# Optimization experiments

Measured on AMD Instinct MI355X. Metric: run time of the kernel, lower is better.

The kernel has to match this reference:

```python
import jax, jax.numpy as jnp
import numpy as np

NUM_Q_HEADS = 32
NUM_KV_HEADS = 8
HEAD_DIM = 128
HIDDEN = 4096
EPS = 1e-6
ROPE_THETA = 1e6


def _rmsnorm(t, w):
    # per-head RMSNorm over last dim (head_dim), as in skip_rmsnorm with residual=None
    var = jnp.mean(t * t, axis=-1, keepdims=True)
    return t * jax.lax.rsqrt(var + EPS) * w


def _rotate_half(t):
    h = t.shape[-1] // 2
    return jnp.concatenate([-t[..., h:], t[..., :h]], axis=-1)


def setup_inputs() -> dict:
    key = jax.random.key(0)
    ks = jax.random.split(key, 4)
    B, S = 2, 1024
    x = jax.random.normal(ks[0], (B, S, HIDDEN), jnp.float32)
    q_proj_w = jax.random.normal(ks[1], (HIDDEN, NUM_Q_HEADS * HEAD_DIM), jnp.float32) * 0.02
    kv_proj_w = jax.random.normal(ks[2], (HIDDEN, 2 * NUM_KV_HEADS * HEAD_DIM), jnp.float32) * 0.02
    o_proj_w = jax.random.normal(ks[3], (NUM_Q_HEADS * HEAD_DIM, HIDDEN), jnp.float32) * 0.02
    q_norm_w = jnp.ones((HEAD_DIM,), jnp.float32)
    k_norm_w = jnp.ones((HEAD_DIM,), jnp.float32)
    # real rotate-half RoPE tables, shape [S, head_dim]
    inv_freq = 1.0 / (ROPE_THETA ** (jnp.arange(0, HEAD_DIM, 2, dtype=jnp.float32) / HEAD_DIM))
    freqs = jnp.arange(S, dtype=jnp.float32)[:, None] * inv_freq[None, :]  # [S, hd/2]
    emb = jnp.concatenate([freqs, freqs], axis=-1)  # [S, hd]
    cos, sin = jnp.cos(emb), jnp.sin(emb)
    kv_buffer = jnp.zeros((16384, 2 * NUM_KV_HEADS, HEAD_DIM), jnp.float32)
    cur_select_index = jnp.arange(B * S, dtype=jnp.int32)
    return {"x": x, "q_proj_w": q_proj_w, "kv_proj_w": kv_proj_w, "o_proj_w": o_proj_w,
            "q_norm_w": q_norm_w, "k_norm_w": k_norm_w, "cos": cos, "sin": sin,
            "kv_buffer": kv_buffer, "cur_select_index": cur_select_index}


def reference(x, q_proj_w, kv_proj_w, o_proj_w, q_norm_w, k_norm_w, cos, sin, kv_buffer, cur_select_index):
    B, S, _ = x.shape
    T = B * S
    xf = x.reshape(T, HIDDEN)
    # projections (weights stored as [in, out])
    xq = (xf @ q_proj_w).reshape(T, NUM_Q_HEADS, HEAD_DIM)
    xkv = xf @ kv_proj_w
    xk = xkv[:, : NUM_KV_HEADS * HEAD_DIM].reshape(T, NUM_KV_HEADS, HEAD_DIM)
    xv = xkv[:, NUM_KV_HEADS * HEAD_DIM:].reshape(T, NUM_KV_HEADS, HEAD_DIM)
    # per-head RMSNorm (Qwen3 q/k norm)
    xq = _rmsnorm(xq, q_norm_w)
    xk = _rmsnorm(xk, k_norm_w)
    # RoPE (cos/sin are [S, hd], tiled over batch, broadcast over heads)
    cos_t = jnp.tile(cos, (B, 1))[:, None, :]  # [T,1,hd]
    sin_t = jnp.tile(sin, (B, 1))[:, None, :]
    xq = xq * cos_t + _rotate_half(xq) * sin_t
    xk = xk * cos_t + _rotate_half(xk) * sin_t
    # paged KV-cache scatter update (update_kv_buffer)
    combined_kv = jnp.concatenate([xk, xv], axis=1)  # [T, 2*Hk, hd]
    buf = kv_buffer.at[cur_select_index].set(combined_kv)
    # ragged causal flash attention (equal per-request lengths here), GQA expand
    rep = NUM_Q_HEADS // NUM_KV_HEADS
    q = xq.reshape(B, S, NUM_Q_HEADS, HEAD_DIM)
    k = jnp.repeat(xk.reshape(B, S, NUM_KV_HEADS, HEAD_DIM), rep, axis=2)
    v = jnp.repeat(xv.reshape(B, S, NUM_KV_HEADS, HEAD_DIM), rep, axis=2)
    scale = HEAD_DIM ** -0.5
    scores = jnp.einsum('bqhd,bkhd->bhqk', q, k) * scale  # [B,H,S,S]
    causal = jnp.tril(jnp.ones((S, S), bool))
    scores = jnp.where(causal[None, None], scores, jnp.float32(-1e30))
    p = jax.nn.softmax(scores, axis=-1)
    attn = jnp.einsum('bhqk,bkhd->bqhd', p, v).reshape(B, S, NUM_Q_HEADS * HEAD_DIM)
    out = attn @ o_proj_w  # [B,S,hidden]
    return out, buf
```

## Files before the change

kernel.cpp:

```cpp
#include <hip/hip_runtime.h>

typedef float fx4 __attribute__((ext_vector_type(4)));
typedef short s16x4 __attribute__((ext_vector_type(4)));
typedef short s16x8 __attribute__((ext_vector_type(8)));
typedef __bf16 bf16x8 __attribute__((ext_vector_type(8)));

__device__ __forceinline__ short f2bf(float f) {
  unsigned u = __builtin_bit_cast(unsigned, f);
  u += 0x7fffu + ((u >> 16) & 1u);
  return (short)(u >> 16);
}

__device__ __forceinline__ bf16x8 ld8(const short* p) {
  s16x8 v = *(const s16x8*)p;
  return __builtin_bit_cast(bf16x8, v);
}

__device__ __forceinline__ void gld16(const void* g, void* l) {
  __builtin_amdgcn_global_load_lds(
      (const __attribute__((address_space(1))) unsigned*)g,
      (__attribute__((address_space(3))) unsigned*)l, 16, 0, 0);
}

template<int N> __device__ __forceinline__ void wait_vmcnt() {
  if constexpr (N == 0)      asm volatile("s_waitcnt vmcnt(0)" ::: "memory");
  else if constexpr (N == 4) asm volatile("s_waitcnt vmcnt(4)" ::: "memory");
  else if constexpr (N == 6) asm volatile("s_waitcnt vmcnt(6)" ::: "memory");
  __builtin_amdgcn_sched_barrier(0);
}

__device__ __forceinline__ void barrier_pin() {
  __builtin_amdgcn_s_barrier();
  __builtin_amdgcn_sched_barrier(0);
}

__global__ __launch_bounds__(256) void cvt_k(const float* __restrict__ in,
                                             short* __restrict__ out) {
  int i = (blockIdx.x * 256 + threadIdx.x) * 8;
  fx4 a = *(const fx4*)(in + i);
  fx4 b = *(const fx4*)(in + i + 4);
  s16x8 w;
  w[0] = f2bf(a[0]); w[1] = f2bf(a[1]); w[2] = f2bf(a[2]); w[3] = f2bf(a[3]);
  w[4] = f2bf(b[0]); w[5] = f2bf(b[1]); w[6] = f2bf(b[2]); w[7] = f2bf(b[3]);
  *(s16x8*)(out + i) = w;
}

__global__ __launch_bounds__(256) void tr_k(const float* __restrict__ in,
    short* __restrict__ out, int K, int N) {
  __shared__ short T[64][72];
  const int ktiles = K >> 6;
  const int tk0 = (blockIdx.x % ktiles) << 6;
  const int tn0 = (blockIdx.x / ktiles) << 6;
  const int tid = threadIdx.x;
  #pragma unroll
  for (int i = 0; i < 4; ++i) {
    int idx = i * 256 + tid;
    int k = idx >> 4, n4 = (idx & 15) << 2;
    fx4 v = *(const fx4*)(in + (size_t)(tk0 + k) * N + tn0 + n4);
    #pragma unroll
    for (int j = 0; j < 4; ++j) T[n4 + j][k] = f2bf(v[j]);
  }
  __syncthreads();
  #pragma unroll
  for (int i = 0; i < 2; ++i) {
    int idx = i * 256 + tid;
    int n = idx >> 3, k8 = (idx & 7) << 3;
    *(s16x8*)(out + (size_t)(tn0 + n) * K + tk0 + k8) = *(const s16x8*)&T[n][k8];
  }
}

__global__ __launch_bounds__(256) void vtr_k(const short* __restrict__ vbp,
                                             short* __restrict__ vbt) {
  __shared__ short T[64][72];
  const int tile = blockIdx.x & 31;
  const int tt = tile & 15, dt = tile >> 4;
  const int bk = blockIdx.x >> 5;
  const int b = bk >> 3, kvh = bk & 7;
  const int t0 = tt << 6, d0 = dt << 6;
  const int tid = threadIdx.x;
  #pragma unroll
  for (int i = 0; i < 2; ++i) {
    int idx = i * 256 + tid;
    int r = idx >> 3, c8 = (idx & 7) << 3;
    s16x8 v = *(const s16x8*)(vbp + (size_t)(b * 1024 + t0 + r) * 1024 + kvh * 128 + d0 + c8);
    #pragma unroll
    for (int j = 0; j < 8; ++j) T[c8 + j][r] = v[j];
  }
  __syncthreads();
  #pragma unroll
  for (int i = 0; i < 2; ++i) {
    int idx = i * 256 + tid;
    int r = idx >> 3, c8 = (idx & 7) << 3;
    *(s16x8*)(vbt + ((size_t)(b * 8 + kvh) * 128 + d0 + r) * 1024 + t0 + c8) =
        *(const s16x8*)&T[r][c8];
  }
}

__global__ __launch_bounds__(512) void gemm8(const short* __restrict__ A,
    const short* __restrict__ Bt, float* __restrict__ Cp, int N, int K) {
  __shared__ short As[2][2][128 * 64];
  __shared__ short Bs[2][2][128 * 64];
  const int tiles_n = N >> 8;
  const int tm = blockIdx.x / tiles_n, tn = blockIdx.x % tiles_n;
  const int tid = threadIdx.x;
  const int lane = tid & 63, wv = tid >> 6;
  const int wm = (wv >> 2) << 6;
  const int wn = (wv & 3) << 5;
  const int r0 = tm << 8, c0 = tn << 8;
  const int lrow = lane & 15, lg = lane >> 4;

  auto stageA = [&](int t, int hh) {
    int k0 = t << 6, s = t & 1;
    #pragma unroll
    for (int i = 0; i < 2; ++i) {
      int c = i * 512 + tid;
      int row = c >> 3, ch = c & 7;
      gld16(A + (size_t)(r0 + hh * 128 + row) * K + k0 + ((ch ^ (row & 7)) << 3),
            &As[s][hh][(i * 512 + wv * 64) * 8]);
    }
  };
  auto stageB = [&](int t, int hh) {
    int k0 = t << 6, s = t & 1;
    #pragma unroll
    for (int i = 0; i < 2; ++i) {
      int c = i * 512 + tid;
      int row = c >> 3, ch = c & 7;
      gld16(Bt + (size_t)(c0 + hh * 128 + row) * K + k0 + ((ch ^ (row & 7)) << 3),
            &Bs[s][hh][(i * 512 + wv * 64) * 8]);
    }
  };

  fx4 acc[2][2][4][2] = {};
  bf16x8 a[4][2], b[2][2];

  auto ldA = [&](int s, int hh) {
    #pragma unroll
    for (int mf = 0; mf < 4; ++mf) {
      int lr = wm + mf * 16 + lrow;
      #pragma unroll
      for (int ks = 0; ks < 2; ++ks)
        a[mf][ks] = ld8(&As[s][hh][lr * 64 + ((((ks << 2) + lg) ^ (lr & 7)) << 3)]);
    }
  };
  auto ldB = [&](int s, int hh) {
    #pragma unroll
    for (int nf = 0; nf < 2; ++nf) {
      int lr = wn + nf * 16 + lrow;
      #pragma unroll
      for (int ks = 0; ks < 2; ++ks)
        b[nf][ks] = ld8(&Bs[s][hh][lr * 64 + ((((ks << 2) + lg) ^ (lr & 7)) << 3)]);
    }
  };

  const int nt = K >> 6;
  stageA(0, 0); stageA(0, 1); stageB(0, 0); stageB(0, 1);
  stageA(1, 0); stageB(1, 1);

  for (int t = 0; t < nt; ++t) {
    const int s = t & 1;
    if (t + 1 < nt) wait_vmcnt<4>(); else wait_vmcnt<0>();
    barrier_pin();
    ldA(s, 0); ldB(s, 0);
    if (t + 1 < nt) stageA(t + 1, 1);
    __builtin_amdgcn_s_setprio(1);
    #pragma unroll
    for (int ks = 0; ks < 2; ++ks)
      #pragma unroll
      for (int mf = 0; mf < 4; ++mf)
        #pragma unroll
        for (int nf = 0; nf < 2; ++nf)
          acc[0][0][mf][nf] = __builtin_amdgcn_mfma_f32_16x16x32_bf16(
              a[mf][ks], b[nf][ks], acc[0][0][mf][nf], 0, 0, 0);
    __builtin_amdgcn_s_setprio(0);
    barrier_pin();
    ldB(s, 1);
    if (t + 1 < nt) stageB(t + 1, 0);
    __builtin_amdgcn_s_setprio(1);
    #pragma unroll
    for (int ks = 0; ks < 2; ++ks)
      #pragma unroll
      for (int mf = 0; mf < 4; ++mf)
        #pragma unroll
        for (int nf = 0; nf < 2; ++nf)
          acc[0][1][mf][nf] = __builtin_amdgcn_mfma_f32_16x16x32_bf16(
              a[mf][ks], b[nf][ks], acc[0][1][mf][nf], 0, 0, 0);
    __builtin_amdgcn_s_setprio(0);
    barrier_pin();
    ldA(s, 1);
    if (t + 2 < nt) stageA(t + 2, 0);
    __builtin_amdgcn_s_setprio(1);
    #pragma unroll
    for (int ks = 0; ks < 2; ++ks)
      #pragma unroll
      for (int mf = 0; mf < 4; ++mf)
        #pragma unroll
        for (int nf = 0; nf < 2; ++nf)
          acc[1][1][mf][nf] = __builtin_amdgcn_mfma_f32_16x16x32_bf16(
              a[mf][ks], b[nf][ks], acc[1][1][mf][nf], 0, 0, 0);
    __builtin_amdgcn_s_setprio(0);
    barrier_pin();
    ldB(s, 0);
    if (t + 2 < nt) stageB(t + 2, 1);
    __builtin_amdgcn_s_setprio(1);
    #pragma unroll
    for (int ks = 0; ks < 2; ++ks)
      #pragma unroll
      for (int mf = 0; mf < 4; ++mf)
        #pragma unroll
        for (int nf = 0; nf < 2; ++nf)
          acc[1][0][mf][nf] = __builtin_amdgcn_mfma_f32_16x16x32_bf16(
              a[mf][ks], b[nf][ks], acc[1][0][mf][nf], 0, 0, 0);
    __builtin_amdgcn_s_setprio(0);
    barrier_pin();
  }
  const int g4 = lg << 2;
  #pragma unroll
  for (int mq = 0; mq < 2; ++mq)
    #pragma unroll
    for (int nq = 0; nq < 2; ++nq)
      #pragma unroll
      for (int mf = 0; mf < 4; ++mf)
        #pragma unroll
        for (int nf = 0; nf < 2; ++nf)
          #pragma unroll
          for (int j = 0; j < 4; ++j) {
            int row = r0 + mq * 128 + wm + mf * 16 + g4 + j;
            int col = c0 + nq * 128 + wn + nf * 16 + lrow;
            Cp[(size_t)row * N + col] = acc[mq][nq][mf][nf][j];
          }
}

__global__ __launch_bounds__(512) void gemm4(const short* __restrict__ A,
    const short* __restrict__ Bt, float* __restrict__ Cp, int N, int K) {
  __shared__ short As[3][2][128 * 64];
  __shared__ short Bs[3][128 * 64];
  const int tiles_n = N >> 7;
  const int tm = blockIdx.x / tiles_n, tn = blockIdx.x % tiles_n;
  const int tid = threadIdx.x;
  const int lane = tid & 63, wv = tid >> 6;
  const int wm = (wv >> 2) << 6;
  const int wn = (wv & 3) << 5;
  const int r0 = tm << 8, c0 = tn << 7;
  const int lrow = lane & 15, lg = lane >> 4;

  auto stageA = [&](int t, int hh) {
    int k0 = t << 6, s = t % 3;
    #pragma unroll
    for (int i = 0; i < 2; ++i) {
      int c = i * 512 + tid;
      int row = c >> 3, ch = c & 7;
      gld16(A + (size_t)(r0 + hh * 128 + row) * K + k0 + ((ch ^ (row & 7)) << 3),
            &As[s][hh][(i * 512 + wv * 64) * 8]);
    }
  };
  auto stageB = [&](int t) {
    int k0 = t << 6, s = t % 3;
    #pragma unroll
    for (int i = 0; i < 2; ++i) {
      int c = i * 512 + tid;
      int row = c >> 3, ch = c & 7;
      gld16(Bt + (size_t)(c0 + row) * K + k0 + ((ch ^ (row & 7)) << 3),
            &Bs[s][(i * 512 + wv * 64) * 8]);
    }
  };

  fx4 acc[2][4][2] = {};
  bf16x8 a[4][2], b[2][2];

  auto ldA = [&](int s, int hh) {
    #pragma unroll
    for (int mf = 0; mf < 4; ++mf) {
      int lr = wm + mf * 16 + lrow;
      #pragma unroll
      for (int ks = 0; ks < 2; ++ks)
        a[mf][ks] = ld8(&As[s][hh][lr * 64 + ((((ks << 2) + lg) ^ (lr & 7)) << 3)]);
    }
  };
  auto ldB = [&](int s) {
    #pragma unroll
    for (int nf = 0; nf < 2; ++nf) {
      int lr = wn + nf * 16 + lrow;
      #pragma unroll
      for (int ks = 0; ks < 2; ++ks)
        b[nf][ks] = ld8(&Bs[s][lr * 64 + ((((ks << 2) + lg) ^ (lr & 7)) << 3)]);
    }
  };

  const int nt = K >> 6;
  stageA(0, 0); stageA(0, 1); stageB(0);
  stageA(1, 0); stageA(1, 1); stageB(1);

  for (int t = 0; t < nt; ++t) {
    const int s = t % 3;
    if (t + 1 < nt) wait_vmcnt<6>(); else wait_vmcnt<0>();
    barrier_pin();
    ldA(s, 0); ldB(s);
    if (t + 2 < nt) stageA(t + 2, 0);
    __builtin_amdgcn_s_setprio(1);
    #pragma unroll
    for (int ks = 0; ks < 2; ++ks)
      #pragma unroll
      for (int mf = 0; mf < 4; ++mf)
        #pragma unroll
        for (int nf = 0; nf < 2; ++nf)
          acc[0][mf][nf] = __builtin_amdgcn_mfma_f32_16x16x32_bf16(
              a[mf][ks], b[nf][ks], acc[0][mf][nf], 0, 0, 0);
    __builtin_amdgcn_s_setprio(0);
    barrier_pin();
    ldA(s, 1);
    if (t + 2 < nt) { stageA(t + 2, 1); stageB(t + 2); }
    __builtin_amdgcn_s_setprio(1);
    #pragma unroll
    for (int ks = 0; ks < 2; ++ks)
      #pragma unroll
      for (int mf = 0; mf < 4; ++mf)
        #pragma unroll
        for (int nf = 0; nf < 2; ++nf)
          acc[1][mf][nf] = __builtin_amdgcn_mfma_f32_16x16x32_bf16(
              a[mf][ks], b[nf][ks], acc[1][mf][nf], 0, 0, 0);
    __builtin_amdgcn_s_setprio(0);
    barrier_pin();
  }
  const int g4 = lg << 2;
  #pragma unroll
  for (int mh = 0; mh < 2; ++mh)
    #pragma unroll
    for (int mf = 0; mf < 4; ++mf)
      #pragma unroll
      for (int nf = 0; nf < 2; ++nf)
        #pragma unroll
        for (int j = 0; j < 4; ++j) {
          int row = r0 + mh * 128 + wm + mf * 16 + g4 + j;
          int col = c0 + wn + nf * 16 + lrow;
          Cp[(size_t)row * N + col] = acc[mh][mf][nf][j];
        }
}

__global__ __launch_bounds__(256) void nr_k(const float* __restrict__ xqkv,
    const float* __restrict__ qnw, const float* __restrict__ knw,
    const float* __restrict__ cosb, const float* __restrict__ sinb,
    const int* __restrict__ idx,
    short* __restrict__ qb, short* __restrict__ kbp, short* __restrict__ vbp,
    float* __restrict__ bufo) {
  int rid = blockIdx.x * 4 + (threadIdx.x >> 6);
  int l = threadIdx.x & 63;
  int type, t, h;
  if (rid < 65536)      { type = 0; t = rid >> 5; h = rid & 31; }
  else if (rid < 81920) { type = 1; int r = rid - 65536; t = r >> 3; h = r & 7; }
  else                  { type = 2; int r = rid - 81920; t = r >> 3; h = r & 7; }
  int s = t & 1023;
  const float* src = xqkv + (size_t)t * 6144 +
                     ((type == 0) ? h * 128 : (type == 1) ? 4096 + h * 128
                                                          : 5120 + h * 128);
  float e0 = src[l], e1 = src[l + 64];
  float out0, out1;
  if (type < 2) {
    float ss = e0 * e0 + e1 * e1;
    #pragma unroll
    for (int off = 1; off < 64; off <<= 1) ss += __shfl_xor(ss, off);
    float r = rsqrtf(ss * (1.0f / 128.0f) + 1e-6f);
    const float* nw = (type == 0) ? qnw : knw;
    float n0 = e0 * r * nw[l], n1 = e1 * r * nw[l + 64];
    float c0 = cosb[s * 128 + l], c1 = cosb[s * 128 + 64 + l];
    float s0 = sinb[s * 128 + l], s1 = sinb[s * 128 + 64 + l];
    out0 = n0 * c0 - n1 * s0;
    out1 = n1 * c1 + n0 * s1;
  } else { out0 = e0; out1 = e1; }
  if (type == 0) {
    short* d = qb + (size_t)t * 4096 + h * 128;
    d[l] = f2bf(out0); d[l + 64] = f2bf(out1);
  } else {
    int br = idx[t];
    float* bd = bufo + (size_t)br * 2048 + (type == 1 ? 0 : 1024) + h * 128;
    bd[l] = out0; bd[l + 64] = out1;
    short* d = (type == 1) ? kbp + (size_t)t * 1024 + h * 128
                           : vbp + (size_t)t * 1024 + h * 128;
    d[l] = f2bf(out0); d[l + 64] = f2bf(out1);
  }
}

#define KLD 136
#define PLD 72

__global__ __launch_bounds__(256) void attn_k(const short* __restrict__ qb,
    const short* __restrict__ kbp, const short* __restrict__ vbt,
    short* __restrict__ ob) {
  __shared__ short Ks[64 * KLD];
  __shared__ short Vs[128 * 64];
  __shared__ short Ps[4][16 * PLD];
  const int bid = blockIdx.x;
  const int qt = 15 - (bid & 15), h = (bid >> 4) & 31, b = bid >> 9;
  const int kvh = h >> 2;
  const int tid = threadIdx.x, lane = tid & 63, w = tid >> 6;
  const int lrow = lane & 15, lg = lane >> 4, lk = lg << 3;
  const int q0 = qt << 6;
  const float SC2 = 0.088388347648318447f * 1.4426950408889634f;

  bf16x8 qf[4];
  {
    const short* qp = qb + ((size_t)(b * 1024 + q0 + w * 16 + lrow) * 32 + h) * 128 + lk;
    #pragma unroll
    for (int kb4 = 0; kb4 < 4; ++kb4) qf[kb4] = ld8(qp + kb4 * 32);
  }

  const short* vt_base = vbt + (size_t)(b * 8 + kvh) * 128 * 1024;

  const int sr = tid >> 4, sd8 = (tid & 15) << 3;
  const int vdr = tid >> 3, vch = tid & 7;
  s16x8 kreg[4], vreg[4];
  auto ldkv = [&](int kv0) {
    #pragma unroll
    for (int it = 0; it < 4; ++it) {
      int r = (it << 4) + sr;
      kreg[it] = *(const s16x8*)(kbp + ((size_t)(b * 1024 + kv0 + r) * 8 + kvh) * 128 + sd8);
      int d = (it << 5) + vdr;
      vreg[it] = *(const s16x8*)(vt_base + (size_t)d * 1024 + kv0 + (vch << 3));
    }
  };
  auto wrkv = [&]() {
    #pragma unroll
    for (int it = 0; it < 4; ++it) {
      int r = (it << 4) + sr;
      *(s16x8*)&Ks[r * KLD + sd8] = kreg[it];
      int d = (it << 5) + vdr;
      *(s16x8*)&Vs[d * 64 + ((vch ^ (d & 7)) << 3)] = vreg[it];
    }
  };

  float m[4], lsum[4];
  fx4 acc[8] = {};
  #pragma unroll
  for (int j = 0; j < 4; ++j) { m[j] = -3.0e38f; lsum[j] = 0.f; }

  ldkv(0);
  wrkv();
  __syncthreads();

  for (int kt = 0; kt <= qt; ++kt) {
    const int kv0 = kt << 6;
    if (kt < qt) ldkv((kt + 1) << 6);
    fx4 sf[4];
    #pragma unroll
    for (int nc = 0; nc < 4; ++nc) {
      fx4 z = {0.f, 0.f, 0.f, 0.f};
      sf[nc] = z;
      #pragma unroll
      for (int kb4 = 0; kb4 < 4; ++kb4) {
        bf16x8 kf = ld8(&Ks[(nc * 16 + lrow) * KLD + kb4 * 32 + lk]);
        sf[nc] = __builtin_amdgcn_mfma_f32_16x16x32_bf16(qf[kb4], kf, sf[nc], 0, 0, 0);
      }
    }
    if (kt == qt) {
      #pragma unroll
      for (int nc = 0; nc < 4; ++nc)
        #pragma unroll
        for (int j = 0; j < 4; ++j) {
          int qr = q0 + w * 16 + (lg << 2) + j;
          int kc = kv0 + nc * 16 + lrow;
          if (kc > qr) sf[nc][j] = -3.0e38f;
        }
    }
    float pm[4];
    #pragma unroll
    for (int j = 0; j < 4; ++j) pm[j] = -3.0e38f;
    #pragma unroll
    for (int nc = 0; nc < 4; ++nc)
      #pragma unroll
      for (int j = 0; j < 4; ++j) pm[j] = fmaxf(pm[j], sf[nc][j]);
    #pragma unroll
    for (int j = 0; j < 4; ++j) {
      pm[j] = fmaxf(pm[j], __shfl_xor(pm[j], 1));
      pm[j] = fmaxf(pm[j], __shfl_xor(pm[j], 2));
      pm[j] = fmaxf(pm[j], __shfl_xor(pm[j], 4));
      pm[j] = fmaxf(pm[j], __shfl_xor(pm[j], 8));
    }
    float alpha[4], rs[4];
    #pragma unroll
    for (int j = 0; j < 4; ++j) {
      float mn = fmaxf(m[j], pm[j]);
      alpha[j] = exp2f((m[j] - mn) * SC2);
      m[j] = mn;
      rs[j] = 0.f;
    }
    #pragma unroll
    for (int nc = 0; nc < 4; ++nc)
      #pragma unroll
      for (int j = 0; j < 4; ++j) {
        float p = exp2f((sf[nc][j] - m[j]) * SC2);
        rs[j] += p;
        Ps[w][((lg << 2) + j) * PLD + nc * 16 + lrow] = f2bf(p);
      }
    #pragma unroll
    for (int j = 0; j < 4; ++j) {
      rs[j] += __shfl_xor(rs[j], 1);
      rs[j] += __shfl_xor(rs[j], 2);
      rs[j] += __shfl_xor(rs[j], 4);
      rs[j] += __shfl_xor(rs[j], 8);
      lsum[j] = lsum[j] * alpha[j] + rs[j];
    }
    #pragma unroll
    for (int dg = 0; dg < 8; ++dg)
      #pragma unroll
      for (int j = 0; j < 4; ++j) acc[dg][j] *= alpha[j];
    #pragma unroll
    for (int kb2 = 0; kb2 < 2; ++kb2) {
      bf16x8 pf = ld8(&Ps[w][lrow * PLD + kb2 * 32 + lk]);
      #pragma unroll
      for (int dg = 0; dg < 8; ++dg) {
        int d = dg * 16 + lrow;
        int tch = (kb2 << 2) + lg;
        bf16x8 vf = ld8(&Vs[d * 64 + ((tch ^ (d & 7)) << 3)]);
        acc[dg] = __builtin_amdgcn_mfma_f32_16x16x32_bf16(pf, vf, acc[dg], 0, 0, 0);
      }
    }
    __syncthreads();
    if (kt < qt) {
      wrkv();
      __syncthreads();
    }
  }
  #pragma unroll
  for (int j = 0; j < 4; ++j) {
    float rl = 1.0f / lsum[j];
    int t = b * 1024 + q0 + w * 16 + (lg << 2) + j;
    short* op = ob + ((size_t)t * 32 + h) * 128;
    #pragma unroll
    for (int dg = 0; dg < 8; ++dg)
      op[dg * 16 + lrow] = f2bf(acc[dg][j] * rl);
  }
}

extern "C" void kernel_launch(void* const* d_in, const int* in_sizes, int n_in,
                              void* d_out, int out_size, void* d_ws, size_t ws_size,
                              hipStream_t stream) {
  (void)in_sizes; (void)n_in; (void)out_size; (void)ws_size;
  const float* x    = (const float*)d_in[0];
  const float* qw   = (const float*)d_in[1];
  const float* kvw  = (const float*)d_in[2];
  const float* ow   = (const float*)d_in[3];
  const float* qnw  = (const float*)d_in[4];
  const float* knw  = (const float*)d_in[5];
  const float* cosb = (const float*)d_in[6];
  const float* sinb = (const float*)d_in[7];
  const float* kvbf = (const float*)d_in[8];
  const int*   idx  = (const int*)d_in[9];

  float* outp = (float*)d_out;
  float* bufp = outp + (size_t)2048 * 4096;

  char* ws = (char*)d_ws;
  float* xqkv = (float*)ws;
  short* qb   = (short*)(ws + (size_t)2048 * 6144 * 4);
  short* kbp  = (short*)((char*)qb + (size_t)2048 * 4096 * 2);
  short* vbp  = (short*)((char*)kbp + (size_t)2048 * 1024 * 2);
  short* attnb = (short*)xqkv;
  short* owt   = (short*)((char*)xqkv + (size_t)2048 * 4096 * 2);
  short* vbt   = owt;

  short* wqkvt = (short*)bufp;
  short* xb    = (short*)((char*)bufp + (size_t)6144 * 4096 * 2);

  cvt_k<<<dim3(4096), dim3(256), 0, stream>>>(x, xb);
  tr_k<<<dim3(64 * 64), dim3(256), 0, stream>>>(qw, wqkvt, 4096, 4096);
  tr_k<<<dim3(64 * 32), dim3(256), 0, stream>>>(kvw, wqkvt + (size_t)4096 * 4096, 4096, 2048);
  gemm8<<<dim3(8 * 24), dim3(512), 0, stream>>>(xb, wqkvt, xqkv, 6144, 4096);
  hipMemcpyAsync(bufp + (size_t)2048 * 2048, kvbf + (size_t)2048 * 2048,
                 (size_t)(16384 - 2048) * 2048 * 4, hipMemcpyDeviceToDevice, stream);
  nr_k<<<dim3(98304 / 4), dim3(256), 0, stream>>>(xqkv, qnw, knw, cosb, sinb, idx,
                                                  qb, kbp, vbp, bufp);
  vtr_k<<<dim3(512), dim3(256), 0, stream>>>(vbp, vbt);
  attn_k<<<dim3(2 * 32 * 16), dim3(256), 0, stream>>>(qb, kbp, vbt, attnb);
  tr_k<<<dim3(64 * 64), dim3(256), 0, stream>>>(ow, owt, 4096, 4096);
  gemm4<<<dim3(8 * 32), dim3(512), 0, stream>>>(attnb, owt, outp, 4096, 4096);
}
```

Baseline: 398.6 us.

## Emit bf16 QKV projection output and double attention query tile per block

The QKV GEMM now writes bf16 instead of fp32, and the norm/RoPE kernel reads it back with a bf16-to-float helper. This halves the intermediate write and read traffic but rounds the pre-norm activations, which also feed the fp32 KV buffer. The attention kernel moves to 512 threads, with each block handling 128 query rows (8 waves) against shared K/V tiles. Each loaded K/V tile is therefore reused by twice as many queries, at the cost of half as many blocks and a causal mask applied on the last two KV tiles. Workspace offsets are rearranged to fit the smaller buffers.

Measured after the change: 385.1 us. 1.03x faster.

```diff
diff --git a/kernel.cpp b/kernel.cpp
--- a/kernel.cpp
+++ b/kernel.cpp
@@ -9,6 +9,10 @@
   unsigned u = __builtin_bit_cast(unsigned, f);
   u += 0x7fffu + ((u >> 16) & 1u);
   return (short)(u >> 16);
+}
+__device__ __forceinline__ float b2f(short s) {
+  unsigned u = ((unsigned)(unsigned short)s) << 16;
+  return __builtin_bit_cast(float, u);
 }
 
 __device__ __forceinline__ bf16x8 ld8(const short* p) {
@@ -96,8 +100,9 @@
   }
 }
 
+template<int BF16OUT>
 __global__ __launch_bounds__(512) void gemm8(const short* __restrict__ A,
-    const short* __restrict__ Bt, float* __restrict__ Cp, int N, int K) {
+    const short* __restrict__ Bt, void* __restrict__ Cp, int N, int K) {
   __shared__ short As[2][2][128 * 64];
   __shared__ short Bs[2][2][128 * 64];
   const int tiles_n = N >> 8;
@@ -226,7 +231,10 @@
           for (int j = 0; j < 4; ++j) {
             int row = r0 + mq * 128 + wm + mf * 16 + g4 + j;
             int col = c0 + nq * 128 + wn + nf * 16 + lrow;
-            Cp[(size_t)row * N + col] = acc[mq][nq][mf][nf][j];
+            if (BF16OUT)
+              ((short*)Cp)[(size_t)row * N + col] = f2bf(acc[mq][nq][mf][nf][j]);
+            else
+              ((float*)Cp)[(size_t)row * N + col] = acc[mq][nq][mf][nf][j];
           }
 }
 
@@ -336,7 +344,7 @@
         }
 }
 
-__global__ __launch_bounds__(256) void nr_k(const float* __restrict__ xqkv,
+__global__ __launch_bounds__(256) void nr_k(const short* __restrict__ xqkv,
     const float* __restrict__ qnw, const float* __restrict__ knw,
     const float* __restrict__ cosb, const float* __restrict__ sinb,
     const int* __restrict__ idx,
@@ -349,10 +357,10 @@
   else if (rid < 81920) { type = 1; int r = rid - 65536; t = r >> 3; h = r & 7; }
   else                  { type = 2; int r = rid - 81920; t = r >> 3; h = r & 7; }
   int s = t & 1023;
-  const float* src = xqkv + (size_t)t * 6144 +
+  const short* src = xqkv + (size_t)t * 6144 +
                      ((type == 0) ? h * 128 : (type == 1) ? 4096 + h * 128
                                                           : 5120 + h * 128);
-  float e0 = src[l], e1 = src[l + 64];
+  float e0 = b2f(src[l]), e1 = b2f(src[l + 64]);
   float out0, out1;
   if (type < 2) {
     float ss = e0 * e0 + e1 * e1;
@@ -382,18 +390,19 @@
 #define KLD 136
 #define PLD 72
 
-__global__ __launch_bounds__(256) void attn_k(const short* __restrict__ qb,
+__global__ __launch_bounds__(512) void attn_k(const short* __restrict__ qb,
     const short* __restrict__ kbp, const short* __restrict__ vbt,
     short* __restrict__ ob) {
   __shared__ short Ks[64 * KLD];
   __shared__ short Vs[128 * 64];
-  __shared__ short Ps[4][16 * PLD];
+  __shared__ short Ps[8][16 * PLD];
   const int bid = blockIdx.x;
-  const int qt = 15 - (bid & 15), h = (bid >> 4) & 31, b = bid >> 9;
+  const int p = 7 - (bid & 7), h = (bid >> 3) & 31, b = bid >> 8;
   const int kvh = h >> 2;
   const int tid = threadIdx.x, lane = tid & 63, w = tid >> 6;
   const int lrow = lane & 15, lg = lane >> 4, lk = lg << 3;
-  const int q0 = qt << 6;
+  const int q0 = p << 7;
+  const int ktmax = 2 * p + 1;
   const float SC2 = 0.088388347648318447f * 1.4426950408889634f;
 
   bf16x8 qf[4];
@@ -405,25 +414,24 @@
 
   const short* vt_base = vbt + (size_t)(b * 8 + kvh) * 128 * 1024;
 
-  const int sr = tid >> 4, sd8 = (tid & 15) << 3;
-  const int vdr = tid >> 3, vch = tid & 7;
-  s16x8 kreg[4], vreg[4];
+  const int sd8 = (tid & 15) << 3;
+  s16x8 kreg[2], vreg[2];
   auto ldkv = [&](int kv0) {
     #pragma unroll
-    for (int it = 0; it < 4; ++it) {
-      int r = (it << 4) + sr;
+    for (int it = 0; it < 2; ++it) {
+      int r = (it << 5) + (tid >> 4);
       kreg[it] = *(const s16x8*)(kbp + ((size_t)(b * 1024 + kv0 + r) * 8 + kvh) * 128 + sd8);
-      int d = (it << 5) + vdr;
-      vreg[it] = *(const s16x8*)(vt_base + (size_t)d * 1024 + kv0 + (vch << 3));
+      int d = (it << 6) + (tid >> 3);
+      vreg[it] = *(const s16x8*)(vt_base + (size_t)d * 1024 + kv0 + ((tid & 7) << 3));
     }
   };
   auto wrkv = [&]() {
     #pragma unroll
-    for (int it = 0; it < 4; ++it) {
-      int r = (it << 4) + sr;
+    for (int it = 0; it < 2; ++it) {
+      int r = (it << 5) + (tid >> 4);
       *(s16x8*)&Ks[r * KLD + sd8] = kreg[it];
-      int d = (it << 5) + vdr;
-      *(s16x8*)&Vs[d * 64 + ((vch ^ (d & 7)) << 3)] = vreg[it];
+      int d = (it << 6) + (tid >> 3);
+      *(s16x8*)&Vs[d * 64 + (((tid & 7) ^ (d & 7)) << 3)] = vreg[it];
     }
   };
 
@@ -436,9 +444,9 @@
   wrkv();
   __syncthreads();
 
-  for (int kt = 0; kt <= qt; ++kt) {
+  for (int kt = 0; kt <= ktmax; ++kt) {
     const int kv0 = kt << 6;
-    if (kt < qt) ldkv((kt + 1) << 6);
+    if (kt < ktmax) ldkv((kt + 1) << 6);
     fx4 sf[4];
     #pragma unroll
     for (int nc = 0; nc < 4; ++nc) {
@@ -450,7 +458,7 @@
         sf[nc] = __builtin_amdgcn_mfma_f32_16x16x32_bf16(qf[kb4], kf, sf[nc], 0, 0, 0);
       }
     }
-    if (kt == qt) {
+    if (kt >= ktmax - 1) {
       #pragma unroll
       for (int nc = 0; nc < 4; ++nc)
         #pragma unroll
@@ -486,9 +494,9 @@
     for (int nc = 0; nc < 4; ++nc)
       #pragma unroll
       for (int j = 0; j < 4; ++j) {
-        float p = exp2f((sf[nc][j] - m[j]) * SC2);
-        rs[j] += p;
-        Ps[w][((lg << 2) + j) * PLD + nc * 16 + lrow] = f2bf(p);
+        float pv = exp2f((sf[nc][j] - m[j]) * SC2);
+        rs[j] += pv;
+        Ps[w][((lg << 2) + j) * PLD + nc * 16 + lrow] = f2bf(pv);
       }
     #pragma unroll
     for (int j = 0; j < 4; ++j) {
@@ -514,7 +522,7 @@
       }
     }
     __syncthreads();
-    if (kt < qt) {
+    if (kt < ktmax) {
       wrkv();
       __syncthreads();
     }
@@ -549,12 +557,12 @@
   float* bufp = outp + (size_t)2048 * 4096;
 
   char* ws = (char*)d_ws;
-  float* xqkv = (float*)ws;
+  short* xqkv = (short*)ws;
   short* qb   = (short*)(ws + (size_t)2048 * 6144 * 4);
   short* kbp  = (short*)((char*)qb + (size_t)2048 * 4096 * 2);
   short* vbp  = (short*)((char*)kbp + (size_t)2048 * 1024 * 2);
-  short* attnb = (short*)xqkv;
-  short* owt   = (short*)((char*)xqkv + (size_t)2048 * 4096 * 2);
+  short* attnb = (short*)(ws + (size_t)2048 * 6144 * 2);
+  short* owt   = (short*)((char*)qb + (size_t)2048 * 4096 * 2 + (size_t)2048 * 2048 * 2 * 2);
   short* vbt   = owt;
 
   short* wqkvt = (short*)bufp;
@@ -563,13 +571,13 @@
   cvt_k<<<dim3(4096), dim3(256), 0, stream>>>(x, xb);
   tr_k<<<dim3(64 * 64), dim3(256), 0, stream>>>(qw, wqkvt, 4096, 4096);
   tr_k<<<dim3(64 * 32), dim3(256), 0, stream>>>(kvw, wqkvt + (size_t)4096 * 4096, 4096, 2048);
-  gemm8<<<dim3(8 * 24), dim3(512), 0, stream>>>(xb, wqkvt, xqkv, 6144, 4096);
+  gemm8<1><<<dim3(8 * 24), dim3(512), 0, stream>>>(xb, wqkvt, (void*)xqkv, 6144, 4096);
   hipMemcpyAsync(bufp + (size_t)2048 * 2048, kvbf + (size_t)2048 * 2048,
                  (size_t)(16384 - 2048) * 2048 * 4, hipMemcpyDeviceToDevice, stream);
   nr_k<<<dim3(98304 / 4), dim3(256), 0, stream>>>(xqkv, qnw, knw, cosb, sinb, idx,
                                                   qb, kbp, vbp, bufp);
   vtr_k<<<dim3(512), dim3(256), 0, stream>>>(vbp, vbt);
-  attn_k<<<dim3(2 * 32 * 16), dim3(256), 0, stream>>>(qb, kbp, vbt, attnb);
+  attn_k<<<dim3(2 * 32 * 8), dim3(512), 0, stream>>>(qb, kbp, vbt, attnb);
   tr_k<<<dim3(64 * 64), dim3(256), 0, stream>>>(ow, owt, 4096, 4096);
   gemm4<<<dim3(8 * 32), dim3(512), 0, stream>>>(attnb, owt, outp, 4096, 4096);
 }
```
